# Kernel tuning notes

Hardware: AMD Instinct MI355X
Metric: run time of the kernel (lower is better)

Reference implementation:

```python
import jax, jax.numpy as jnp
import numpy as np

BSZ, D = 64, 65536
N_NODES, N_FEATS, EMBED_DIM = 1024, 256, 256


def setup_inputs() -> dict:
    key = jax.random.key(0)
    k1, k2, k3, k4, k5, k6 = jax.random.split(key, 6)
    flat_inputs = jax.random.normal(k1, (BSZ, D), dtype=jnp.float32)
    node_ids = jax.random.randint(k2, (BSZ, D), 0, N_NODES, dtype=jnp.int64 if jax.config.jax_enable_x64 else jnp.int32)
    feat_ids = jax.random.randint(k3, (BSZ, D), 0, N_FEATS, dtype=jnp.int64 if jax.config.jax_enable_x64 else jnp.int32)
    # Linear(n_feats -> embed_dim): W is (embed_dim, n_feats) like torch, plus bias.
    lim = 1.0 / np.sqrt(N_FEATS)
    W = jax.random.uniform(k4, (EMBED_DIM, N_FEATS), minval=-lim, maxval=lim, dtype=jnp.float32)
    b = jax.random.uniform(k5, (EMBED_DIM,), minval=-lim, maxval=lim, dtype=jnp.float32)
    global_emb = jax.random.normal(k6, (N_NODES, EMBED_DIM), dtype=jnp.float32)
    return {"flat_inputs": flat_inputs, "node_ids": node_ids, "feat_ids": feat_ids,
            "W": W, "b": b, "global_emb": global_emb}


def _expand(vals, node_ids, feat_ids, n_nodes, n_feats):
    # scatter-fill a dense (bsz, n_nodes, n_feats) tensor (zeros elsewhere)
    bsz, d = vals.shape
    batch_ids = jnp.broadcast_to(jnp.arange(bsz)[:, None], (bsz, d))
    out = jnp.zeros((bsz, n_nodes, n_feats), dtype=vals.dtype)
    return out.at[batch_ids.ravel(), node_ids.ravel(), feat_ids.ravel()].set(vals.ravel())


def reference(flat_inputs, node_ids, feat_ids, W, b, global_emb):
    obs_mat = _expand(flat_inputs, node_ids, feat_ids, N_NODES, N_FEATS)
    mask_mat = _expand(jnp.ones_like(flat_inputs), node_ids, feat_ids, N_NODES, N_FEATS)
    obs_counts = mask_mat.sum(-1, keepdims=True)            # (bsz, n_nodes, 1)
    obs_masked = jnp.nan_to_num((obs_mat * mask_mat) / obs_counts)
    missing_node_mask = obs_counts == 0
    # nodewise Linear + global embedding broadcast over batch
    embedded = jnp.einsum('bnf,ef->bne', obs_masked, W) + b + global_emb[None, :, :]
    return embedded, missing_node_mask
```

## Files before the change

### kernel.cpp

```cpp
#include <hip/hip_runtime.h>
#include <hip/hip_bf16.h>

#define BSZ    64
#define DLEN   65536
#define NNODES 1024
#define NFEATS 256
#define EDIM   256
#define NROWS  (BSZ * NNODES)

#define NRANGE  16
#define NBUCKET (BSZ * NRANGE)
#define NSLICE  16
#define SCAP    368
#define WPAD    268
#define CW      132
#define TW      260

typedef __bf16 bf16x8 __attribute__((ext_vector_type(8)));
typedef float  f32x4  __attribute__((ext_vector_type(4)));

__device__ __forceinline__ unsigned short f2bf(float x) {
  union { float f; unsigned u; } c; c.f = x;
  unsigned r = c.u + 0x7FFFu + ((c.u >> 16) & 1u);
  return (unsigned short)(r >> 16);
}

__global__ __launch_bounds__(1024, 8) void bucket_kernel(
    const float* __restrict__ x, const int* __restrict__ nid,
    const int* __restrict__ fid, unsigned* __restrict__ scnt,
    uint2* __restrict__ gbuf,
    const float* __restrict__ W, unsigned short* __restrict__ Wb) {
  __shared__ uint2 lbuf[NRANGE][SCAP];
  __shared__ unsigned lcnt[NRANGE];

  const int t = threadIdx.x;
  if (t < NRANGE) lcnt[t] = 0;

  if (blockIdx.x < 16) {
    int wi = (blockIdx.x * 1024 + t) * 4;
    float4 w = *(const float4*)(W + wi);
    ushort4 o;
    o.x = f2bf(w.x); o.y = f2bf(w.y); o.z = f2bf(w.z); o.w = f2bf(w.w);
    *(ushort4*)(Wb + wi) = o;
  }
  __syncthreads();

  const int b = blockIdx.x >> 4;
  const int k = blockIdx.x & 15;
  const int i = blockIdx.x * 4096 + t * 4;

  float4 xv = *(const float4*)(x + i);
  int4   nv = *(const int4*)(nid + i);
  int4   fv = *(const int4*)(fid + i);
  int   nd[4] = {nv.x, nv.y, nv.z, nv.w};
  int   ft[4] = {fv.x, fv.y, fv.z, fv.w};
  float vl[4] = {xv.x, xv.y, xv.z, xv.w};
#pragma unroll
  for (int j = 0; j < 4; ++j) {
    int d = (i + j) & 0xFFFF;
    unsigned pack = (((unsigned)(d + 1)) << 15) | ((unsigned)f2bf(vl[j]) >> 1);
    int r = nd[j] >> 6;
    unsigned row = (unsigned)(nd[j] & 63);
    uint2 rec;
    rec.x = pack;
    rec.y = row * WPAD + (unsigned)ft[j];
    unsigned li = atomicAdd(&lcnt[r], 1u);
    if (li < SCAP) lbuf[r][li] = rec;
  }
  __syncthreads();

  const int wv = t >> 6, lane = t & 63;
  unsigned n = lcnt[wv]; if (n > SCAP) n = SCAP;
  uint2* dst = gbuf + ((size_t)(b * NRANGE + wv) * NSLICE + k) * SCAP;
  for (unsigned j = lane; j < n; j += 64) dst[j] = lbuf[wv][j];
  if (lane == 0) scnt[(b * NRANGE + wv) * NSLICE + k] = n;
}

__global__ __launch_bounds__(1024, 8) void fused_kernel(
    const unsigned* __restrict__ scnt, const uint2* __restrict__ gbuf,
    const unsigned short* __restrict__ Wb, const float* __restrict__ bias,
    const float* __restrict__ gemb,
    float* __restrict__ out_emb, float* __restrict__ out_mask) {
  __shared__ __align__(16) unsigned win[64 * WPAD];
  __shared__ float scl[64];

  const int t = threadIdx.x;
  const int g = blockIdx.x;
  const int row0 = g * 64;
  const int nb = (g & 15) * 64;
  const int wv = t >> 6, lane = t & 63;

  unsigned cn = scnt[g * NSLICE + wv];
  const uint2* sl = gbuf + ((size_t)g * NSLICE + wv) * SCAP;
  const uint4* s4 = (const uint4*)sl;
  int np = (int)(cn >> 1);
  uint4 r0, r1, r2;
  bool v0 = lane < np, v1 = lane + 64 < np, v2 = lane + 128 < np;
  if (v0) r0 = s4[lane];
  if (v1) r1 = s4[lane + 64];
  if (v2) r2 = s4[lane + 128];

#pragma unroll
  for (int k = 0; k < 4; ++k) {
    int idx = t + k * 1024;
    *(uint4*)&win[(idx >> 6) * WPAD + (idx & 63) * 4] = make_uint4(0u, 0u, 0u, 0u);
  }
  __syncthreads();

  if (v0) { atomicMax(&win[r0.y & 0xFFFFu], r0.x); atomicMax(&win[r0.w & 0xFFFFu], r0.z); }
  if (v1) { atomicMax(&win[r1.y & 0xFFFFu], r1.x); atomicMax(&win[r1.w & 0xFFFFu], r1.z); }
  if (v2) { atomicMax(&win[r2.y & 0xFFFFu], r2.x); atomicMax(&win[r2.w & 0xFFFFu], r2.z); }
  if ((cn & 1u) && lane == 0) {
    uint2 rec = sl[cn - 1];
    atomicMax(&win[rec.y & 0xFFFFu], rec.x);
  }
  __syncthreads();

  const int lr  = t >> 4;
  const int seg = t & 15;
  uint4 rg[4];
  {
    const uint4* rowp = (const uint4*)&win[lr * WPAD];
    int c = 0;
#pragma unroll
    for (int j = 0; j < 4; ++j) {
      rg[j] = rowp[seg + 16 * j];
      c += (rg[j].x != 0u) + (rg[j].y != 0u) + (rg[j].z != 0u) + (rg[j].w != 0u);
    }
    c += __shfl_down(c, 8, 16);
    c += __shfl_down(c, 4, 16);
    c += __shfl_down(c, 2, 16);
    c += __shfl_down(c, 1, 16);
    if (seg == 0) {
      scl[lr] = c ? 1.0f / (float)c : 0.0f;
      out_mask[row0 + lr] = c ? 0.0f : 1.0f;
    }
  }
  __syncthreads();

#pragma unroll
  for (int j = 0; j < 4; ++j) {
    unsigned w0 = ((rg[j].x & 0x7FFFu) << 1) | ((rg[j].y & 0x7FFFu) << 17);
    unsigned w1 = ((rg[j].z & 0x7FFFu) << 1) | ((rg[j].w & 0x7FFFu) << 17);
    *(uint2*)&win[lr * CW + (seg + 16 * j) * 2] = make_uint2(w0, w1);
  }
  __syncthreads();

  const int cl   = lane & 15;
  const int q    = lane >> 4;
  const int col  = wv * 16 + cl;

  f32x4 acc[4];
#pragma unroll
  for (int mt = 0; mt < 4; ++mt) acc[mt] = (f32x4)(0.0f);

#pragma unroll
  for (int ks = 0; ks < 8; ++ks) {
    bf16x8 bfr = __builtin_bit_cast(bf16x8,
        *(const uint4*)(Wb + (size_t)col * NFEATS + ks * 32 + q * 8));
#pragma unroll
    for (int mt = 0; mt < 4; ++mt) {
      bf16x8 afr = __builtin_bit_cast(bf16x8,
          *(const uint4*)&win[(mt * 16 + cl) * CW + ks * 16 + q * 4]);
      acc[mt] = __builtin_amdgcn_mfma_f32_16x16x32_bf16(afr, bfr, acc[mt], 0, 0, 0);
    }
  }
  __syncthreads();

  {
    float* winf = (float*)win;
#pragma unroll
    for (int mt = 0; mt < 4; ++mt) {
#pragma unroll
      for (int r2i = 0; r2i < 4; ++r2i) {
        int row = mt * 16 + q * 4 + r2i;
        winf[row * TW + col] = acc[mt][r2i] * scl[row];
      }
    }
  }
  __syncthreads();

  {
    const float* winf = (const float*)win;
#pragma unroll
    for (int k = 0; k < 4; ++k) {
      int f = t + k * 1024;
      int row = f >> 6, cg = (f & 63) * 4;
      float4 a  = *(const float4*)&winf[row * TW + cg];
      float4 gv = *(const float4*)&gemb[(size_t)(nb + row) * EDIM + cg];
      float4 bv = *(const float4*)&bias[cg];
      float4 o;
      o.x = a.x + bv.x + gv.x;
      o.y = a.y + bv.y + gv.y;
      o.z = a.z + bv.z + gv.z;
      o.w = a.w + bv.w + gv.w;
      *(float4*)&out_emb[(size_t)(row0 + row) * EDIM + cg] = o;
    }
  }
}

extern "C" void kernel_launch(void* const* d_in, const int* in_sizes, int n_in,
                              void* d_out, int out_size, void* d_ws, size_t ws_size,
                              hipStream_t stream) {
  const float* x    = (const float*)d_in[0];
  const int*   nid  = (const int*)d_in[1];
  const int*   fid  = (const int*)d_in[2];
  const float* W    = (const float*)d_in[3];
  const float* bias = (const float*)d_in[4];
  const float* gemb = (const float*)d_in[5];

  float* out_emb  = (float*)d_out;
  float* out_mask = out_emb + (size_t)NROWS * EDIM;

  unsigned* scnt = (unsigned*)d_ws;
  uint2* gbuf = (uint2*)((char*)d_ws + 65536);
  unsigned short* Wb = (unsigned short*)((char*)d_ws + 65536 +
                        (size_t)NBUCKET * NSLICE * SCAP * sizeof(uint2));

  bucket_kernel<<<(BSZ * DLEN) / 4096, 1024, 0, stream>>>(x, nid, fid, scnt, gbuf, W, Wb);
  fused_kernel<<<NBUCKET, 1024, 0, stream>>>(scnt, gbuf, Wb, bias, gemb, out_emb, out_mask);
}
```

Measured before the change: 144.0 us.

## Halve node rows per bucket and use 512-thread fused blocks

Node ranges are split into 32-row buckets instead of 64. The fused kernel now runs 2048 blocks of 512 threads, each wave scattering two slices and computing a 2x2 MFMA tile over 32 columns. Slice capacity and the workspace offsets are resized to match. The smaller LDS window per block is meant to let more blocks stay resident per CU and spread the work more evenly. In exchange the bucket kernel's LDS staging grows and the weight matrix is read twice as often overall.

```diff
diff --git a/kernel.cpp b/kernel.cpp
--- a/kernel.cpp
+++ b/kernel.cpp
@@ -8,13 +8,14 @@
 #define EDIM   256
 #define NROWS  (BSZ * NNODES)
 
-#define NRANGE  16
+#define NRANGE  32
 #define NBUCKET (BSZ * NRANGE)
 #define NSLICE  16
-#define SCAP    368
+#define SCAP    208
 #define WPAD    268
 #define CW      132
 #define TW      260
+#define HROWS   32
 
 typedef __bf16 bf16x8 __attribute__((ext_vector_type(8)));
 typedef float  f32x4  __attribute__((ext_vector_type(4)));
@@ -59,8 +60,8 @@
   for (int j = 0; j < 4; ++j) {
     int d = (i + j) & 0xFFFF;
     unsigned pack = (((unsigned)(d + 1)) << 15) | ((unsigned)f2bf(vl[j]) >> 1);
-    int r = nd[j] >> 6;
-    unsigned row = (unsigned)(nd[j] & 63);
+    int r = nd[j] >> 5;
+    unsigned row = (unsigned)(nd[j] & 31);
     uint2 rec;
     rec.x = pack;
     rec.y = row * WPAD + (unsigned)ft[j];
@@ -70,49 +71,63 @@
   __syncthreads();
 
   const int wv = t >> 6, lane = t & 63;
-  unsigned n = lcnt[wv]; if (n > SCAP) n = SCAP;
-  uint2* dst = gbuf + ((size_t)(b * NRANGE + wv) * NSLICE + k) * SCAP;
-  for (unsigned j = lane; j < n; j += 64) dst[j] = lbuf[wv][j];
-  if (lane == 0) scnt[(b * NRANGE + wv) * NSLICE + k] = n;
-}
-
-__global__ __launch_bounds__(1024, 8) void fused_kernel(
+#pragma unroll
+  for (int rr = 0; rr < 2; ++rr) {
+    int r = wv * 2 + rr;
+    unsigned n = lcnt[r]; if (n > SCAP) n = SCAP;
+    uint2* dst = gbuf + ((size_t)(b * NRANGE + r) * NSLICE + k) * SCAP;
+    for (unsigned j = lane; j < n; j += 64) dst[j] = lbuf[r][j];
+    if (lane == 0) scnt[(b * NRANGE + r) * NSLICE + k] = n;
+  }
+}
+
+__global__ __launch_bounds__(512, 8) void fused_kernel(
     const unsigned* __restrict__ scnt, const uint2* __restrict__ gbuf,
     const unsigned short* __restrict__ Wb, const float* __restrict__ bias,
     const float* __restrict__ gemb,
     float* __restrict__ out_emb, float* __restrict__ out_mask) {
-  __shared__ __align__(16) unsigned win[64 * WPAD];
-  __shared__ float scl[64];
+  __shared__ __align__(16) unsigned win[HROWS * WPAD];
+  __shared__ float scl[HROWS];
 
   const int t = threadIdx.x;
   const int g = blockIdx.x;
-  const int row0 = g * 64;
-  const int nb = (g & 15) * 64;
+  const int row0 = g * HROWS;
+  const int nb = (g & 31) * HROWS;
   const int wv = t >> 6, lane = t & 63;
 
-  unsigned cn = scnt[g * NSLICE + wv];
-  const uint2* sl = gbuf + ((size_t)g * NSLICE + wv) * SCAP;
-  const uint4* s4 = (const uint4*)sl;
-  int np = (int)(cn >> 1);
-  uint4 r0, r1, r2;
-  bool v0 = lane < np, v1 = lane + 64 < np, v2 = lane + 128 < np;
-  if (v0) r0 = s4[lane];
-  if (v1) r1 = s4[lane + 64];
-  if (v2) r2 = s4[lane + 128];
+  const int s0 = g * NSLICE + wv * 2;
+  unsigned cn0 = scnt[s0], cn1 = scnt[s0 + 1];
+  const uint2* sl0 = gbuf + (size_t)s0 * SCAP;
+  const uint2* sl1 = sl0 + SCAP;
+  const uint4* p0 = (const uint4*)sl0;
+  const uint4* p1 = (const uint4*)sl1;
+  int np0 = (int)(cn0 >> 1), np1 = (int)(cn1 >> 1);
+  uint4 a0, a1, b0, b1;
+  bool va0 = lane < np0, va1 = lane + 64 < np0;
+  bool vb0 = lane < np1, vb1 = lane + 64 < np1;
+  if (va0) a0 = p0[lane];
+  if (va1) a1 = p0[lane + 64];
+  if (vb0) b0 = p1[lane];
+  if (vb1) b1 = p1[lane + 64];
 
 #pragma unroll
   for (int k = 0; k < 4; ++k) {
-    int idx = t + k * 1024;
+    int idx = t + k * 512;
     *(uint4*)&win[(idx >> 6) * WPAD + (idx & 63) * 4] = make_uint4(0u, 0u, 0u, 0u);
   }
   __syncthreads();
 
-  if (v0) { atomicMax(&win[r0.y & 0xFFFFu], r0.x); atomicMax(&win[r0.w & 0xFFFFu], r0.z); }
-  if (v1) { atomicMax(&win[r1.y & 0xFFFFu], r1.x); atomicMax(&win[r1.w & 0xFFFFu], r1.z); }
-  if (v2) { atomicMax(&win[r2.y & 0xFFFFu], r2.x); atomicMax(&win[r2.w & 0xFFFFu], r2.z); }
-  if ((cn & 1u) && lane == 0) {
-    uint2 rec = sl[cn - 1];
-    atomicMax(&win[rec.y & 0xFFFFu], rec.x);
+  if (va0) { atomicMax(&win[a0.y], a0.x); atomicMax(&win[a0.w], a0.z); }
+  if (va1) { atomicMax(&win[a1.y], a1.x); atomicMax(&win[a1.w], a1.z); }
+  if (vb0) { atomicMax(&win[b0.y], b0.x); atomicMax(&win[b0.w], b0.z); }
+  if (vb1) { atomicMax(&win[b1.y], b1.x); atomicMax(&win[b1.w], b1.z); }
+  if ((cn0 & 1u) && lane == 0) {
+    uint2 rec = sl0[cn0 - 1];
+    atomicMax(&win[rec.y], rec.x);
+  }
+  if ((cn1 & 1u) && lane == 1) {
+    uint2 rec = sl1[cn1 - 1];
+    atomicMax(&win[rec.y], rec.x);
   }
   __syncthreads();
 
@@ -148,21 +163,29 @@
 
   const int cl   = lane & 15;
   const int q    = lane >> 4;
-  const int col  = wv * 16 + cl;
-
-  f32x4 acc[4];
-#pragma unroll
-  for (int mt = 0; mt < 4; ++mt) acc[mt] = (f32x4)(0.0f);
+  const int col0 = wv * 32;
+
+  f32x4 acc[2][2];
+#pragma unroll
+  for (int mt = 0; mt < 2; ++mt)
+#pragma unroll
+    for (int nt = 0; nt < 2; ++nt) acc[mt][nt] = (f32x4)(0.0f);
 
 #pragma unroll
   for (int ks = 0; ks < 8; ++ks) {
-    bf16x8 bfr = __builtin_bit_cast(bf16x8,
-        *(const uint4*)(Wb + (size_t)col * NFEATS + ks * 32 + q * 8));
-#pragma unroll
-    for (int mt = 0; mt < 4; ++mt) {
+    bf16x8 bfr[2];
+#pragma unroll
+    for (int nt = 0; nt < 2; ++nt) {
+      bfr[nt] = __builtin_bit_cast(bf16x8,
+          *(const uint4*)(Wb + (size_t)(col0 + nt * 16 + cl) * NFEATS + ks * 32 + q * 8));
+    }
+#pragma unroll
+    for (int mt = 0; mt < 2; ++mt) {
       bf16x8 afr = __builtin_bit_cast(bf16x8,
           *(const uint4*)&win[(mt * 16 + cl) * CW + ks * 16 + q * 4]);
-      acc[mt] = __builtin_amdgcn_mfma_f32_16x16x32_bf16(afr, bfr, acc[mt], 0, 0, 0);
+#pragma unroll
+      for (int nt = 0; nt < 2; ++nt)
+        acc[mt][nt] = __builtin_amdgcn_mfma_f32_16x16x32_bf16(afr, bfr[nt], acc[mt][nt], 0, 0, 0);
     }
   }
   __syncthreads();
@@ -170,11 +193,15 @@
   {
     float* winf = (float*)win;
 #pragma unroll
-    for (int mt = 0; mt < 4; ++mt) {
-#pragma unroll
-      for (int r2i = 0; r2i < 4; ++r2i) {
-        int row = mt * 16 + q * 4 + r2i;
-        winf[row * TW + col] = acc[mt][r2i] * scl[row];
+    for (int nt = 0; nt < 2; ++nt) {
+      int col = col0 + nt * 16 + cl;
+#pragma unroll
+      for (int mt = 0; mt < 2; ++mt) {
+#pragma unroll
+        for (int r2i = 0; r2i < 4; ++r2i) {
+          int row = mt * 16 + q * 4 + r2i;
+          winf[row * TW + col] = acc[mt][nt][r2i] * scl[row];
+        }
       }
     }
   }
@@ -184,7 +211,7 @@
     const float* winf = (const float*)win;
 #pragma unroll
     for (int k = 0; k < 4; ++k) {
-      int f = t + k * 1024;
+      int f = t + k * 512;
       int row = f >> 6, cg = (f & 63) * 4;
       float4 a  = *(const float4*)&winf[row * TW + cg];
       float4 gv = *(const float4*)&gemb[(size_t)(nb + row) * EDIM + cg];
@@ -213,10 +240,10 @@
   float* out_mask = out_emb + (size_t)NROWS * EDIM;
 
   unsigned* scnt = (unsigned*)d_ws;
-  uint2* gbuf = (uint2*)((char*)d_ws + 65536);
-  unsigned short* Wb = (unsigned short*)((char*)d_ws + 65536 +
+  uint2* gbuf = (uint2*)((char*)d_ws + 131072);
+  unsigned short* Wb = (unsigned short*)((char*)d_ws + 131072 +
                         (size_t)NBUCKET * NSLICE * SCAP * sizeof(uint2));
 
   bucket_kernel<<<(BSZ * DLEN) / 4096, 1024, 0, stream>>>(x, nid, fid, scnt, gbuf, W, Wb);
-  fused_kernel<<<NBUCKET, 1024, 0, stream>>>(scnt, gbuf, Wb, bias, gemb, out_emb, out_mask);
-}
+  fused_kernel<<<NBUCKET, 512, 0, stream>>>(scnt, gbuf, Wb, bias, gemb, out_emb, out_mask);
+}
```

Result: slower. 155.6 us (+8.1%).
